# Performance work log

Hardware: AMD Instinct MI355X
Metric: run time of the kernel (lower is better)

Reference implementation:

```python
import jax, jax.numpy as jnp
import numpy as np

B, H, N = 2, 4, 8192
K = 32       # sub_size
TEMP = 2.0   # temperature for the soft permutation indicator


def setup_inputs() -> dict:
    key = jax.random.key(0)
    ranking = jax.random.normal(key, (B, H, N, 1), dtype=jnp.float32)
    return {"ranking": ranking, "i": 0, "j": N}


@jax.custom_vjp
def hsigmoid(x):
    # Hard step indicator (x > 0) with straight-through gradient (CoCN Hsigmoid)
    return (x > 0).astype(x.dtype)

def _hs_fwd(x):
    return hsigmoid(x), None

def _hs_bwd(res, g):
    return (g,)

hsigmoid.defvjp(_hs_fwd, _hs_bwd)


def _windows(x, n, k):
    # circular pad last dim by k-1, then unfold into sliding windows of size k
    xp = jnp.concatenate([x, x[..., :k - 1]], axis=-1)
    idx = jnp.arange(n)[:, None] + jnp.arange(k)[None, :]   # (n, k)
    return xp[..., idx]                                      # (..., n, k)


def reference(ranking, i, j):
    b, h, n = ranking.shape[:3]
    k = K
    r = ranking[..., 0]                                      # (b,h,n)
    order = jnp.argsort(r, axis=2, stable=True)              # (b,h,n) stable sort indices
    r_sorted = jnp.take_along_axis(r, order, axis=2)

    val_win = _windows(r_sorted, n, k)                       # (b,h,n,k)
    idx_win = _windows(order.astype(jnp.float32), n, k).astype(jnp.int32)

    # scatter windows back to original node order == gather by inverse permutation
    inv = jnp.argsort(order, axis=2)                         # (b,h,n)
    val_win = jnp.take_along_axis(val_win, inv[..., None], axis=2)
    idx_win = jnp.take_along_axis(idx_win, inv[..., None], axis=2)

    # within each window, sort by original node index (stable), reorder values alike
    k_order = jnp.argsort(idx_win, axis=-1, stable=True)
    sorted_idx = jnp.take_along_axis(idx_win, k_order, axis=-1)
    val_win = jnp.take_along_axis(val_win, k_order, axis=-1)

    # slice node window [i, i+j)
    val_win = val_win[:, :, i:i + j]                         # (b,h,j,k)
    sorted_idx = sorted_idx[:, :, i:i + j]

    # (b,j,h,k) -> (b*j, h, k, 1)
    x = jnp.transpose(val_win, (0, 2, 1, 3)).reshape(-1, h, k, 1)
    rel = x - jnp.swapaxes(x, -1, -2)                        # (b*j,h,k,k)
    tie_bias = jnp.triu((rel == 0).astype(jnp.float32), 1)   # break ties above diagonal
    rel = rel + tie_bias
    uni = hsigmoid(jax.nn.relu(rel))                         # 1 where strictly greater
    rank = jnp.sum(uni, axis=-2, keepdims=True)              # (b*j,h,1,k)

    ind = jnp.arange(k, dtype=jnp.float32)[:, None] - rank   # (b*j,h,k,k)
    ind = jnp.where(ind < 0, ind + k, ind)
    perm = jnp.exp(-ind * TEMP)
    return perm, sorted_idx
```

## Files before the change

### kernel.cpp

```cpp
#include <hip/hip_runtime.h>
#include <stdint.h>

#define B_ 2
#define H_ 4
#define N_ 8192
#define K_ 32
#define ROWS 8
#define NTOT (ROWS * N_)
#define PERM_ELEMS ((size_t)B_ * N_ * H_ * K_ * K_)

#define JT 512
#define EPT 4
#define NJT 16

typedef float f32x4 __attribute__((ext_vector_type(4)));

__device__ __forceinline__ uint32_t mono(float f) {
    uint32_t u = __float_as_uint(f);
    return (u & 0x80000000u) ? ~u : (u | 0x80000000u);
}

__global__ __launch_bounds__(256) void rank_count(const float* __restrict__ ranking,
                                                  int* __restrict__ partial) {
    __shared__ uint64_t jk[JT];
    const int blk = blockIdx.x;
    const int jt  = blk & 15;
    const int it  = (blk >> 4) & 7;
    const int row = blk >> 7;
    const float* rr = ranking + (size_t)row * N_;

    for (int j = threadIdx.x; j < JT; j += 256) {
        const int jj = jt * JT + j;
        jk[j] = ((uint64_t)mono(rr[jj]) << 13) | (uint32_t)jj;
    }

    uint64_t my[EPT];
    const int ibase = it * (EPT * 256) + threadIdx.x;
    #pragma unroll
    for (int e = 0; e < EPT; ++e) {
        const int ii = ibase + e * 256;
        my[e] = ((uint64_t)mono(rr[ii]) << 13) | (uint32_t)ii;
    }
    __syncthreads();

    int cnt[EPT] = {0, 0, 0, 0};
    const ulonglong2* jv = (const ulonglong2*)jk;
    for (int j = 0; j < JT / 2; j += 2) {
        const ulonglong2 a = jv[j];
        const ulonglong2 b = jv[j + 1];
        #pragma unroll
        for (int e = 0; e < EPT; ++e) {
            cnt[e] += (a.x < my[e]);
            cnt[e] += (a.y < my[e]);
            cnt[e] += (b.x < my[e]);
            cnt[e] += (b.y < my[e]);
        }
    }
    #pragma unroll
    for (int e = 0; e < EPT; ++e)
        partial[(size_t)jt * NTOT + (size_t)row * N_ + ibase + e * 256] = cnt[e];
}

__global__ __launch_bounds__(256) void scatter_sorted(const float* __restrict__ ranking,
                                                      const int* __restrict__ partial,
                                                      int2* __restrict__ vid) {
    const int g = blockIdx.x * 256 + threadIdx.x;
    const int row = g >> 13;
    int s = 0;
    #pragma unroll
    for (int jt = 0; jt < NJT; ++jt) s += partial[(size_t)jt * NTOT + g];
    vid[(size_t)row * N_ + s] = make_int2(__float_as_int(ranking[g]), g & (N_ - 1));
}

__global__ __launch_bounds__(256) void windows_kernel(
    const int2* __restrict__ vid,
    float* __restrict__ perm_out,
    float* __restrict__ idx_out)
{
    __shared__ int2 vt[64];
    __shared__ uint64_t wk[8][K_];
    __shared__ float4 cinfo[8][K_];

    const int tid = threadIdx.x;
    const int row = blockIdx.x >> 8;
    const int t0  = (blockIdx.x & 255) * 32;

    for (int q = tid; q < 64; q += 256) {
        int sidx = t0 + q; if (sidx >= N_) sidx -= N_;
        vt[q] = vid[(size_t)row * N_ + sidx];
    }
    __syncthreads();

    const int wave = tid >> 6;
    const int lane = tid & 63;
    const int half = lane >> 5;
    const int m    = lane & 31;
    const int ws   = wave * 2 + half;
    const int b    = row >> 2;
    const int h    = row & 3;

    const float EM2  = 0.13533528f;
    const float EM4  = 0.018315639f;
    const float EM8  = 3.3546262e-4f;
    const float EM16 = 1.12535175e-7f;
    const float E64C = 1.6038108e-28f;

    for (int iter = 0; iter < 4; ++iter) {
        const int q = iter * 8 + ws;
        const int2 vi = vt[q + m];
        const int id = vi.y;
        const int rid = (N_ - 1) - id;
        const uint64_t key2 =
            ((uint64_t)mono(__int_as_float(vi.x)) << 13) | (uint32_t)rid;

        wk[ws][m] = key2;
        __builtin_amdgcn_wave_barrier();

        int rank = 0, pos = 0;
        #pragma unroll
        for (int p = 0; p < K_; ++p) {
            const uint64_t kp = wk[ws][p];
            rank += (kp > key2);
            pos  += ((int)((uint32_t)kp & (uint32_t)(N_ - 1)) > rid);
        }

        cinfo[ws][pos] = make_float4(__expf(2.0f * (float)rank),
                                     __int_as_float(rank), (float)id, 0.0f);
        __builtin_amdgcn_wave_barrier();

        {
            const int n = vt[q].y;
            __builtin_nontemporal_store(
                cinfo[ws][m].z,
                &idx_out[((size_t)row * N_ + n) * K_ + m]);
        }
        __builtin_amdgcn_wave_barrier();

        #pragma unroll
        for (int win = 0; win < 2; ++win) {
            const int slot = wave * 2 + win;
            const int qq2  = iter * 8 + slot;
            const int n    = vt[qq2].y;
            f32x4* pout =
                (f32x4*)(perm_out + (((size_t)b * N_ + n) * H_ + h) * (K_ * K_));

            const int j0 = (lane & 7) * 4;
            const float4 c0 = cinfo[slot][j0 + 0];
            const float4 c1 = cinfo[slot][j0 + 1];
            const float4 c2 = cinfo[slot][j0 + 2];
            const float4 c3 = cinfo[slot][j0 + 3];
            const int r0 = __float_as_int(c0.y), r1 = __float_as_int(c1.y);
            const int r2 = __float_as_int(c2.y), r3 = __float_as_int(c3.y);

            const int mrow = lane >> 3;
            float a = (mrow & 1 ? EM2 : 1.0f) *
                      (mrow & 2 ? EM4 : 1.0f) *
                      (mrow & 4 ? EM8 : 1.0f);
            int mm = mrow;

            #pragma unroll
            for (int qq = 0; qq < 4; ++qq) {
                f32x4 val;
                val.x = a * c0.x * (mm < r0 ? E64C : 1.0f);
                val.y = a * c1.x * (mm < r1 ? E64C : 1.0f);
                val.z = a * c2.x * (mm < r2 ? E64C : 1.0f);
                val.w = a * c3.x * (mm < r3 ? E64C : 1.0f);
                __builtin_nontemporal_store(val, &pout[qq * 64 + lane]);
                a *= EM16;
                mm += 8;
            }
        }
        __builtin_amdgcn_wave_barrier();
    }
}

extern "C" void kernel_launch(void* const* d_in, const int* in_sizes, int n_in,
                              void* d_out, int out_size, void* d_ws, size_t ws_size,
                              hipStream_t stream) {
    const float* ranking = (const float*)d_in[0];

    char* ws = (char*)d_ws;
    int*  partial = (int*)ws;
    int2* vid     = (int2*)(ws + 4 * 1024 * 1024);

    float* perm_out = (float*)d_out;
    float* idx_out  = perm_out + PERM_ELEMS;

    hipLaunchKernelGGL(rank_count, dim3(1024), dim3(256), 0, stream,
                       ranking, partial);
    hipLaunchKernelGGL(scatter_sorted, dim3(NTOT / 256), dim3(256), 0, stream,
                       ranking, partial, vid);
    hipLaunchKernelGGL(windows_kernel, dim3(2048), dim3(256), 0, stream,
                       vid, perm_out, idx_out);
}
```

Measured before the change: 319.4 us.

## Iterate windows in output node order via inverse permutation for coalesced writes

```diff
diff --git a/kernel.cpp b/kernel.cpp
--- a/kernel.cpp
+++ b/kernel.cpp
@@ -63,41 +63,39 @@
 
 __global__ __launch_bounds__(256) void scatter_sorted(const float* __restrict__ ranking,
                                                       const int* __restrict__ partial,
-                                                      int2* __restrict__ vid) {
+                                                      int2* __restrict__ vid,
+                                                      int* __restrict__ inv) {
     const int g = blockIdx.x * 256 + threadIdx.x;
     const int row = g >> 13;
     int s = 0;
     #pragma unroll
     for (int jt = 0; jt < NJT; ++jt) s += partial[(size_t)jt * NTOT + g];
     vid[(size_t)row * N_ + s] = make_int2(__float_as_int(ranking[g]), g & (N_ - 1));
+    inv[g] = s;
 }
 
 __global__ __launch_bounds__(256) void windows_kernel(
     const int2* __restrict__ vid,
+    const int* __restrict__ inv,
     float* __restrict__ perm_out,
     float* __restrict__ idx_out)
 {
-    __shared__ int2 vt[64];
     __shared__ uint64_t wk[8][K_];
     __shared__ float4 cinfo[8][K_];
 
-    const int tid = threadIdx.x;
-    const int row = blockIdx.x >> 8;
-    const int t0  = (blockIdx.x & 255) * 32;
-
-    for (int q = tid; q < 64; q += 256) {
-        int sidx = t0 + q; if (sidx >= N_) sidx -= N_;
-        vt[q] = vid[(size_t)row * N_ + sidx];
-    }
-    __syncthreads();
+    const int tid   = threadIdx.x;
+    const int blk   = blockIdx.x;
+    const int h     = blk & 3;
+    const int ntile = (blk >> 2) & 255;
+    const int b     = blk >> 10;
+    const int row   = b * 4 + h;
+    const int n0    = ntile * 32;
 
     const int wave = tid >> 6;
     const int lane = tid & 63;
     const int half = lane >> 5;
     const int m    = lane & 31;
     const int ws   = wave * 2 + half;
-    const int b    = row >> 2;
-    const int h    = row & 3;
 
     const float EM2  = 0.13533528f;
     const float EM4  = 0.018315639f;
@@ -106,8 +104,11 @@
     const float E64C = 1.6038108e-28f;
 
     for (int iter = 0; iter < 4; ++iter) {
-        const int q = iter * 8 + ws;
-        const int2 vi = vt[q + m];
+        const int q  = iter * 8 + ws;
+        const int n  = n0 + q;
+        const int s0 = inv[(size_t)row * N_ + n];
+        const int sp = (s0 + m) & (N_ - 1);
+        const int2 vi = vid[(size_t)row * N_ + sp];
         const int id = vi.y;
         const int rid = (N_ - 1) - id;
         const uint64_t key2 =
@@ -128,21 +129,17 @@
                                      __int_as_float(rank), (float)id, 0.0f);
         __builtin_amdgcn_wave_barrier();
 
-        {
-            const int n = vt[q].y;
-            __builtin_nontemporal_store(
-                cinfo[ws][m].z,
-                &idx_out[((size_t)row * N_ + n) * K_ + m]);
-        }
+        __builtin_nontemporal_store(
+            cinfo[ws][m].z,
+            &idx_out[((size_t)row * N_ + n) * K_ + m]);
         __builtin_amdgcn_wave_barrier();
 
         #pragma unroll
         for (int win = 0; win < 2; ++win) {
             const int slot = wave * 2 + win;
-            const int qq2  = iter * 8 + slot;
-            const int n    = vt[qq2].y;
+            const int n2   = n0 + iter * 8 + slot;
             f32x4* pout =
-                (f32x4*)(perm_out + (((size_t)b * N_ + n) * H_ + h) * (K_ * K_));
+                (f32x4*)(perm_out + (((size_t)b * N_ + n2) * H_ + h) * (K_ * K_));
 
             const int j0 = (lane & 7) * 4;
             const float4 c0 = cinfo[slot][j0 + 0];
@@ -182,6 +179,7 @@
     char* ws = (char*)d_ws;
     int*  partial = (int*)ws;
     int2* vid     = (int2*)(ws + 4 * 1024 * 1024);
+    int*  inv     = (int*)(ws + 4 * 1024 * 1024 + 512 * 1024);
 
     float* perm_out = (float*)d_out;
     float* idx_out  = perm_out + PERM_ELEMS;
@@ -189,7 +187,7 @@
     hipLaunchKernelGGL(rank_count, dim3(1024), dim3(256), 0, stream,
                        ranking, partial);
     hipLaunchKernelGGL(scatter_sorted, dim3(NTOT / 256), dim3(256), 0, stream,
-                       ranking, partial, vid);
+                       ranking, partial, vid, inv);
     hipLaunchKernelGGL(windows_kernel, dim3(2048), dim3(256), 0, stream,
-                       vid, perm_out, idx_out);
+                       vid, inv, perm_out, idx_out);
 }
```

New measurement: 315.7 us. No clear change (-1.1%).
